# Optimization experiments

Hardware: AMD Instinct MI355X
Metric: run time of the kernel (lower is better)

## Reference

```python
import jax, jax.numpy as jnp
import numpy as np

D_MODEL = 16
NHEAD = 4
HEAD_DIM = D_MODEL // NHEAD
DFF = 64
NUM_LAYERS = 2
LN_EPS = 1e-5


def _layer_norm(x, w, b):
    mu = jnp.mean(x, axis=-1, keepdims=True)
    var = jnp.mean(jnp.square(x - mu), axis=-1, keepdims=True)
    return (x - mu) * jax.lax.rsqrt(var + LN_EPS) * w + b


def _encoder_layer(x, Wqkv, bqkv, Wo, bo, ln1w, ln1b, W1, b1, W2, b2, ln2w, ln2b):
    # x: [N, T, D]  (post-norm TransformerEncoderLayer, ReLU, no dropout)
    N, T, D = x.shape
    qkv = x @ Wqkv.T + bqkv                      # [N, T, 3D]
    q, k, v = jnp.split(qkv, 3, axis=-1)
    q = q.reshape(N, T, NHEAD, HEAD_DIM)
    k = k.reshape(N, T, NHEAD, HEAD_DIM)
    v = v.reshape(N, T, NHEAD, HEAD_DIM)
    scale = 1.0 / np.sqrt(HEAD_DIM)
    logits = jnp.einsum('nthd,nshd->nhts', q, k) * scale   # [N, H, T, T]
    attn = jax.nn.softmax(logits, axis=-1)
    ctx = jnp.einsum('nhts,nshd->nthd', attn, v).reshape(N, T, D)
    attn_out = ctx @ Wo.T + bo
    x = _layer_norm(x + attn_out, ln1w, ln1b)
    ff = jax.nn.relu(x @ W1.T + b1) @ W2.T + b2
    x = _layer_norm(x + ff, ln2w, ln2b)
    return x


def setup_inputs() -> dict:
    key = jax.random.key(0)
    ks = jax.random.split(key, 20)
    B, T, H, W = 1, 24, 256, 256
    L = NUM_LAYERS
    s = 0.05
    inp = {
        'x': jax.random.normal(ks[0], (B, T, H, W), dtype=jnp.float32),
        'Win': jax.random.normal(ks[1], (D_MODEL, 1), dtype=jnp.float32) * s,
        'bin': jnp.zeros((D_MODEL,), jnp.float32),
        'Wqkv': jax.random.normal(ks[2], (L, 3 * D_MODEL, D_MODEL), jnp.float32) * s,
        'bqkv': jnp.zeros((L, 3 * D_MODEL), jnp.float32),
        'Wo': jax.random.normal(ks[3], (L, D_MODEL, D_MODEL), jnp.float32) * s,
        'bo': jnp.zeros((L, D_MODEL), jnp.float32),
        'ln1w': jnp.ones((L, D_MODEL), jnp.float32),
        'ln1b': jnp.zeros((L, D_MODEL), jnp.float32),
        'W1': jax.random.normal(ks[4], (L, DFF, D_MODEL), jnp.float32) * s,
        'b1': jnp.zeros((L, DFF), jnp.float32),
        'W2': jax.random.normal(ks[5], (L, D_MODEL, DFF), jnp.float32) * s,
        'b2': jnp.zeros((L, D_MODEL), jnp.float32),
        'ln2w': jnp.ones((L, D_MODEL), jnp.float32),
        'ln2b': jnp.zeros((L, D_MODEL), jnp.float32),
        'Wout': jax.random.normal(ks[6], (1, D_MODEL), jnp.float32) * s,
        'bout': jnp.zeros((1,), jnp.float32),
    }
    return inp


def reference(x, Win, bin, Wqkv, bqkv, Wo, bo, ln1w, ln1b, W1, b1, W2, b2, ln2w, ln2b, Wout, bout):
    B, T, H, W = x.shape
    h = x.transpose(0, 2, 3, 1).reshape(B * H * W, T, 1)
    h = h @ Win.T + bin                              # [N, T, D]
    for l in range(NUM_LAYERS):
        h = _encoder_layer(h, Wqkv[l], bqkv[l], Wo[l], bo[l], ln1w[l], ln1b[l],
                           W1[l], b1[l], W2[l], b2[l], ln2w[l], ln2b[l])
    h = h @ Wout.T + bout                            # [N, T, 1]
    return h.reshape(B, H, W, T).transpose(0, 3, 1, 2)
```

## Files before the change

kernel.cpp:

```cpp
#include <hip/hip_runtime.h>
#include <hip/hip_bf16.h>


#define DM 16
#define NH 4
#define HD 4
#define TT 24
#define DFF 64
#define NSEQ 65536
#define SPB 8
#define BLK 192

typedef __fp16 h2_t  __attribute__((ext_vector_type(2)));
typedef __fp16 f16x4 __attribute__((ext_vector_type(4)));
typedef __fp16 f16x8 __attribute__((ext_vector_type(8)));
typedef float  f32x4 __attribute__((ext_vector_type(4)));

#define MFMA16(A,B,C) __builtin_amdgcn_mfma_f32_16x16x16f16(A,B,C,0,0,0)
#define LGKM0 asm volatile("s_waitcnt lgkmcnt(0)" ::: "memory")

#define OFF_WIN  0
#define OFF_BIN  16
#define OFF_WQKV 32
#define OFF_BQKV 1568
#define OFF_WO   1664
#define OFF_BO   2176
#define OFF_LN1W 2208
#define OFF_LN1B 2240
#define OFF_B1   2272
#define OFF_B2   2400
#define OFF_LN2W 2432
#define OFF_LN2B 2464
#define OFF_WOUT 2496
#define OFF_BOUT 2512
#define OFF_WQH  2516
#define OFF_WOH  3284
#define OFF_W1H  3540
#define OFF_W2H  4564
#define OFF_XBF  5588
#define OFF_DA   5592
#define OFF_WV   5608
#define OFF_W0   5672
#define NDW      5688

#define FOLD 0.7213475204444817f

#define KVS 97
#define TSTR 40

__device__ __forceinline__ float fdot2(h2_t a, h2_t b, float c) {
    return __builtin_amdgcn_fdot2(a, b, c, false);
}
__device__ __forceinline__ h2_t pkrn(float a, float b) {
    h2_t r; r[0] = (__fp16)a; r[1] = (__fp16)b; return r;
}

__device__ __forceinline__ int x_is_bf16(const unsigned* xw) {
    int ok = 1;
    #pragma unroll
    for (int i = 0; i < 32; ++i) {
        unsigned u = xw[i];
        unsigned e0 = (u >> 7)  & 0xFF;
        unsigned e1 = (u >> 23) & 0xFF;
        ok &= (e0 >= 64u) & (e0 <= 134u) & (e1 >= 64u) & (e1 <= 134u);
    }
    return ok;
}

__global__ __launch_bounds__(256) void cvt_params(
    const void* __restrict__ p0,  const void* __restrict__ p1,
    const void* __restrict__ p2,  const void* __restrict__ p3,
    const void* __restrict__ p4,  const void* __restrict__ p5,
    const void* __restrict__ p6,  const void* __restrict__ p7,
    const void* __restrict__ p8,  const void* __restrict__ p9,
    const void* __restrict__ p10, const void* __restrict__ p11,
    const void* __restrict__ p12, const void* __restrict__ p13,
    const void* __restrict__ p14, const void* __restrict__ p15,
    const void* __restrict__ px,
    float* __restrict__ ws)
{
    int i = blockIdx.x * 256 + threadIdx.x;
    if (i >= NDW) return;
    const int wbf = (((const unsigned*)p6)[0] == 0x3F803F80u);
    auto ld = [&](const void* p, int j) -> float {
        return wbf ? __bfloat162float(((const __hip_bfloat16*)p)[j])
                   : ((const float*)p)[j];
    };
    unsigned* wsu = (unsigned*)ws;
    auto st2 = [&](float a, float b) {
        union { h2_t h; unsigned u; } cv;
        cv.h = pkrn(a, b);
        wsu[i] = cv.u;
    };

    if      (i < OFF_BIN)  { ws[i] = ld(p0, i); }
    else if (i < OFF_WQKV) { ws[i] = ld(p1, i - OFF_BIN); }
    else if (i < OFF_BQKV) {
        int k = i - OFF_WQKV;
        int row = (k >> 4) % 48;
        float v = ld(p2, k);
        if (row < DM) v *= FOLD;
        ws[i] = v;
    }
    else if (i < OFF_WO) {
        int k = i - OFF_BQKV;
        float v = ld(p3, k);
        if (k % 48 < DM) v *= FOLD;
        ws[i] = v;
    }
    else if (i < OFF_BO)   { ws[i] = ld(p4,  i - OFF_WO);   }
    else if (i < OFF_LN1W) { ws[i] = ld(p5,  i - OFF_BO);   }
    else if (i < OFF_LN1B) { ws[i] = ld(p6,  i - OFF_LN1W); }
    else if (i < OFF_B1)   { ws[i] = ld(p7,  i - OFF_LN1B); }
    else if (i < OFF_B2)   { ws[i] = ld(p9,  i - OFF_B1);   }
    else if (i < OFF_LN2W) { ws[i] = ld(p11, i - OFF_B2);   }
    else if (i < OFF_LN2B) { ws[i] = ld(p12, i - OFF_LN2W); }
    else if (i < OFF_WOUT) { ws[i] = ld(p13, i - OFF_LN2B); }
    else if (i < OFF_BOUT) { ws[i] = ld(p14, i - OFF_WOUT); }
    else if (i < OFF_WQH)  { ws[i] = ld(p15, 0); }
    else if (i < OFF_WOH) {
        int k = i - OFF_WQH, l = k / 384, r = (k % 384) / 8, dp = k % 8;
        int j = l * 768 + r * 16 + 2 * dp;
        float s = (r < DM) ? FOLD : 1.f;
        st2(ld(p2, j) * s, ld(p2, j + 1) * s);
    }
    else if (i < OFF_W1H) {
        int k = i - OFF_WOH, l = k / 128, o = (k % 128) / 8, dp = k % 8;
        int j = l * 256 + o * 16 + 2 * dp;
        st2(ld(p4, j), ld(p4, j + 1));
    }
    else if (i < OFF_W2H) {
        int k = i - OFF_W1H, l = k / 512, f = (k % 512) / 8, dp = k % 8;
        int j = l * 1024 + f * 16 + 2 * dp;
        st2(ld(p8, j), ld(p8, j + 1));
    }
    else if (i < OFF_XBF) {
        int k = i - OFF_W2H, l = k / 512, r = k % 512, o = r / 32, fp = r % 32;
        int j = l * 1024 + o * 64 + 2 * fp;
        st2(ld(p10, j), ld(p10, j + 1));
    }
    else if (i < OFF_DA) {
        ws[i] = (i == OFF_XBF) ? (x_is_bf16((const unsigned*)px) ? 1.f : 0.f)
                               : 0.f;
    }
    else if (i < OFF_WV) {
        int k = i - OFF_DA, kind = k >> 2, hh = k & 3;
        float acc = 0.f;
        for (int j = hh * 4; j < hh * 4 + 4; ++j) {
            float qv;
            if (kind < 2) {
                qv = 0.f;
                for (int m = 0; m < 16; ++m) qv += ld(p2, j*16 + m) * ld(p0, m);
            } else {
                qv = ld(p3, j);
                for (int m = 0; m < 16; ++m) qv += ld(p2, j*16 + m) * ld(p1, m);
            }
            float kv;
            if ((kind & 1) == 0) {
                kv = 0.f;
                for (int m = 0; m < 16; ++m) kv += ld(p2, (16+j)*16 + m) * ld(p0, m);
            } else {
                kv = ld(p3, 16 + j);
                for (int m = 0; m < 16; ++m) kv += ld(p2, (16+j)*16 + m) * ld(p1, m);
            }
            acc += qv * kv;
        }
        ws[i] = acc * FOLD;
    }
    else if (i < OFF_W0) {
        int k = i - OFF_WV, o = k >> 2, hh = k & 3;
        float acc = 0.f;
        for (int j = hh * 4; j < hh * 4 + 4; ++j) {
            float vd = 0.f;
            for (int m = 0; m < 16; ++m) vd += ld(p2, (32+j)*16 + m) * ld(p0, m);
            acc += ld(p4, o*16 + j) * vd;
        }
        ws[i] = acc;
    }
    else {
        int o = i - OFF_W0;
        float acc = ld(p5, o);
        for (int j = 0; j < 16; ++j) {
            float vo = ld(p3, 32 + j);
            for (int m = 0; m < 16; ++m) vo += ld(p2, (32+j)*16 + m) * ld(p1, m);
            acc += ld(p4, o*16 + j) * vo;
        }
        ws[i] = acc;
    }
}


__device__ __forceinline__ void attn4(const float4* k4, const float4* v4,
                                      int base, const float* q, float* ctx) {
    #pragma unroll
    for (int hh = 0; hh < NH; ++hh) {
        const float qa = q[hh*4+0], qb = q[hh*4+1];
        const float qc = q[hh*4+2], qd = q[hh*4+3];
        float sum = 0.f, cx = 0.f, cy = 0.f, cz = 0.f, cw = 0.f;
        #pragma unroll
        for (int s = 0; s < TT; ++s) {
            float4 kk = k4[base + s * NH + hh];
            float e = __builtin_exp2f(qa*kk.x + qb*kk.y + qc*kk.z + qd*kk.w);
            float4 vv = v4[base + s * NH + hh];
            sum += e;
            cx += e*vv.x; cy += e*vv.y; cz += e*vv.z; cw += e*vv.w;
        }
        float inv = __builtin_amdgcn_rcpf(sum);
        ctx[hh*4+0] = cx*inv; ctx[hh*4+1] = cy*inv;
        ctx[hh*4+2] = cz*inv; ctx[hh*4+3] = cw*inv;
    }
}

__device__ __forceinline__ void ln16(const float* y, const float* w,
                                     const float* b, float* out) {
    float mu = 0.f;
    #pragma unroll
    for (int o = 0; o < DM; ++o) mu += y[o];
    mu *= (1.f / DM);
    float var = 0.f;
    #pragma unroll
    for (int o = 0; o < DM; ++o) { float z = y[o] - mu; var += z * z; }
    float r = rsqrtf(var * (1.f / DM) + 1e-5f);
    #pragma unroll
    for (int o = 0; o < DM; ++o) out[o] = (y[o] - mu) * r * w[o] + b[o];
}

__device__ __forceinline__ void stage_hi(const float* v, __fp16* slab, int lane) {
    #pragma unroll
    for (int m = 0; m < 4; ++m) {
        f16x4 p;
        #pragma unroll
        for (int j = 0; j < 4; ++j) p[j] = (__fp16)v[4*m+j];
        *(f16x4*)(slab + lane * TSTR + m * 8) = p;
    }
}

__device__ __forceinline__ void wo1(float* h, const float* ctx,
        const __fp16* Wh, const float* bo, const float* lw, const float* lb,
        __fp16* slab, int col, int grp, int lane)
{
    stage_hi(ctx, slab, lane);
    LGKM0;
    f16x4 B[4];
    #pragma unroll
    for (int m = 0; m < 4; ++m)
        B[m] = *(const f16x4*)(slab + (m*16 + col) * TSTR + grp * 8);
    LGKM0;
    f16x4 A = *(const f16x4*)(Wh + col * DM + grp * 4);
    f32x4 C = *(const f32x4*)(bo + grp * 4);
    #pragma unroll
    for (int m = 0; m < 4; ++m) {
        f32x4 d = MFMA16(A, B[m], C);
        f16x4 o4;
        #pragma unroll
        for (int j = 0; j < 4; ++j) o4[j] = (__fp16)d[j];
        *(f16x4*)(slab + (m*16 + col) * TSTR + grp * 8 + 4) = o4;
    }
    LGKM0;
    float y[DM];
    #pragma unroll
    for (int m = 0; m < 4; ++m) {
        f16x4 a = *(const f16x4*)(slab + lane * TSTR + m * 8 + 4);
        #pragma unroll
        for (int j = 0; j < 4; ++j) y[4*m+j] = h[4*m+j] + (float)a[j];
    }
    ln16(y, lw, lb, h);
}

__device__ __forceinline__ void ff_mfma(float* h, int col, int grp, int lane,
        const __fp16* W1h,
        const __fp16* W2h,
        const float* b1, const float* b2,
        const float* l2w, const float* l2b,
        __fp16* slab)
{
    stage_hi(h, slab, lane);
    LGKM0;
    f16x4 B1[4];
    #pragma unroll
    for (int m = 0; m < 4; ++m)
        B1[m] = *(const f16x4*)(slab + (m*16 + col) * TSTR + grp * 8);
    LGKM0;
    f16x4 A1[4], A2[4];
    f32x4 bb1[4];
    #pragma unroll
    for (int c = 0; c < 4; ++c) {
        A1[c]  = *(const f16x4*)(W1h + (c*16 + col)*16 + grp*4);
        A2[c]  = *(const f16x4*)(W2h + col*64 + c*16 + grp*4);
        bb1[c] = *(const f32x4*)(b1 + c*16 + grp*4);
    }
    const f32x4 b2f = *(const f32x4*)(b2 + grp*4);
    #pragma unroll
    for (int m = 0; m < 4; ++m) {
        f32x4 d1[4];
        #pragma unroll
        for (int c = 0; c < 4; ++c) d1[c] = MFMA16(A1[c], B1[m], bb1[c]);
        f16x4 u[4];
        #pragma unroll
        for (int c = 0; c < 4; ++c) {
            #pragma unroll
            for (int j = 0; j < 4; ++j)
                u[c][j] = (__fp16)fmaxf(d1[c][j], 0.f);
        }
        f32x4 d2 = b2f;
        #pragma unroll
        for (int c = 0; c < 4; ++c) d2 = MFMA16(A2[c], u[c], d2);
        f16x4 o4;
        #pragma unroll
        for (int j = 0; j < 4; ++j) o4[j] = (__fp16)d2[j];
        *(f16x4*)(slab + (m*16 + col) * TSTR + grp * 8 + 4) = o4;
    }
    LGKM0;
    float y[DM];
    #pragma unroll
    for (int m = 0; m < 4; ++m) {
        f16x4 a = *(const f16x4*)(slab + lane * TSTR + m * 8 + 4);
        #pragma unroll
        for (int j = 0; j < 4; ++j)
            y[4*m+j] = h[4*m+j] + (float)a[j];
    }
    ln16(y, l2w, l2b, h);
}

__global__ __launch_bounds__(BLK, 3) void tf_kernel(
    const void* __restrict__ xin,
    const float* __restrict__ P,
    void* __restrict__ outp)
{
    __shared__ float4 kvbuf[2 * SPB * KVS];
    __shared__ float  xs[SPB * 25];
    float4* k4 = kvbuf;
    float4* v4 = kvbuf + SPB * KVS;

    const __fp16* WqkvH = (const __fp16*)(P + OFF_WQH);
    const __fp16* WoHh  = (const __fp16*)(P + OFF_WOH);
    const __fp16* W1h   = (const __fp16*)(P + OFF_W1H);
    const __fp16* W2h   = (const __fp16*)(P + OFF_W2H);

    const int tid  = threadIdx.x;
    const int sl   = tid / TT;
    const int t    = tid % TT;
    const int n    = blockIdx.x * SPB + sl;
    const int idx  = t * NSEQ + n;
    const int base = sl * KVS;
    const int lane = tid & 63;
    const int wb   = tid & ~63;
    const int col  = lane & 15;
    const int grp  = lane >> 4;

    __fp16* slab = (__fp16*)kvbuf + (tid >> 6) * (64 * TSTR);

    const int xbf = (P[OFF_XBF] != 0.f);

    float xv;
    if (xbf) xv = __bfloat162float(((const __hip_bfloat16*)xin)[idx]);
    else     xv = ((const float*)xin)[idx];
    xs[sl * 25 + t] = xv;

    float h[DM];
    #pragma unroll
    for (int d = 0; d < DM; ++d)
        h[d] = xv * P[OFF_WIN + d] + P[OFF_BIN + d];
    __syncthreads();

    {
        float m1[NH];
        #pragma unroll
        for (int hh = 0; hh < NH; ++hh) {
            float f1 = P[OFF_DA + hh]     * xv + P[OFF_DA + 8  + hh];
            float f2 = P[OFF_DA + 4 + hh] * xv + P[OFF_DA + 12 + hh];
            float sum = 0.f, sxv = 0.f;
            #pragma unroll
            for (int s = 0; s < TT; ++s) {
                float xvs = xs[sl * 25 + s];
                float e = __builtin_exp2f(f1 * xvs + f2);
                sum += e;
                sxv += e * xvs;
            }
            m1[hh] = sxv * __builtin_amdgcn_rcpf(sum);
        }
        float y[DM];
        #pragma unroll
        for (int o = 0; o < DM; ++o) {
            f32x4 wv = *(const f32x4*)(P + OFF_WV + o * 4);
            y[o] = h[o] + P[OFF_W0 + o]
                 + m1[0]*wv[0] + m1[1]*wv[1] + m1[2]*wv[2] + m1[3]*wv[3];
        }
        ln16(y, P + OFF_LN1W, P + OFF_LN1B, h);

        ff_mfma(h, col, grp, lane, W1h, W2h,
                P + OFF_B1, P + OFF_B2, P + OFF_LN2W, P + OFF_LN2B, slab);
    }

    {
        const __fp16* WqH1 = WqkvH + 768;
        const float*  bq   = P + OFF_BQKV + 48;

        stage_hi(h, slab, lane);
        LGKM0;
        f16x4 B[4];
        #pragma unroll
        for (int m = 0; m < 4; ++m)
            B[m] = *(const f16x4*)(slab + (m*16 + col) * TSTR + grp * 8);
        f16x4 Ak = *(const f16x4*)(WqH1 + (16 + col) * DM + grp * 4);
        f16x4 Av = *(const f16x4*)(WqH1 + (32 + col) * DM + grp * 4);
        f32x4 Ck = *(const f32x4*)(bq + 16 + grp * 4);
        f32x4 Cv = *(const f32x4*)(bq + 32 + grp * 4);
        f32x4 dk[4], dv[4];
        #pragma unroll
        for (int m = 0; m < 4; ++m) {
            dk[m] = MFMA16(Ak, B[m], Ck);
            dv[m] = MFMA16(Av, B[m], Cv);
        }
        __syncthreads();
        #pragma unroll
        for (int m = 0; m < 4; ++m) {
            int bt = wb + m * 16 + col;
            int s2 = bt / TT, t2 = bt - s2 * TT;
            int ad = s2 * KVS + t2 * NH + grp;
            k4[ad] = make_float4(dk[m][0], dk[m][1], dk[m][2], dk[m][3]);
            v4[ad] = make_float4(dv[m][0], dv[m][1], dv[m][2], dv[m][3]);
        }

        h2_t h2[8];
        #pragma unroll
        for (int m = 0; m < 8; ++m) h2[m] = pkrn(h[2*m], h[2*m+1]);
        float q[DM];
        #pragma unroll
        for (int m = 0; m < 8; ++m) {
            float a0 = bq[2*m], a1 = bq[2*m+1];
            const h2_t* w0 = (const h2_t*)(WqH1 + (2*m) * DM);
            const h2_t* w1 = (const h2_t*)(WqH1 + (2*m+1) * DM);
            #pragma unroll
            for (int dp = 0; dp < 8; ++dp) {
                a0 = fdot2(h2[dp], w0[dp], a0);
                a1 = fdot2(h2[dp], w1[dp], a1);
            }
            q[2*m] = a0; q[2*m+1] = a1;
        }
        __syncthreads();

        float ctx[DM];
        attn4(k4, v4, base, q, ctx);
        __syncthreads();

        wo1(h, ctx, WoHh + 256, P + OFF_BO + 16,
            P + OFF_LN1W + 16, P + OFF_LN1B + 16, slab, col, grp, lane);

        ff_mfma(h, col, grp, lane, W1h + 1024, W2h + 1024,
                P + OFF_B1 + 64, P + OFF_B2 + 16,
                P + OFF_LN2W + 16, P + OFF_LN2B + 16, slab);
    }

    float a = P[OFF_BOUT];
    #pragma unroll
    for (int d = 0; d < DM; ++d)
        a += h[d] * P[OFF_WOUT + d];
    if (xbf) ((__hip_bfloat16*)outp)[idx] = __float2bfloat16(a);
    else     ((float*)outp)[idx] = a;
}

extern "C" void kernel_launch(void* const* d_in, const int* in_sizes, int n_in,
                              void* d_out, int out_size, void* d_ws, size_t ws_size,
                              hipStream_t stream) {
    float* P = (float*)d_ws;

    cvt_params<<<(NDW + 255) / 256, 256, 0, stream>>>(
        d_in[1],  d_in[2],  d_in[3],  d_in[4],
        d_in[5],  d_in[6],  d_in[7],  d_in[8],
        d_in[9],  d_in[10], d_in[11], d_in[12],
        d_in[13], d_in[14], d_in[15], d_in[16],
        d_in[0],
        P);

    tf_kernel<<<NSEQ / SPB, BLK, 0, stream>>>(d_in[0], P, d_out);
}
```

Baseline: 275.3 us.

## Store layer-2 K/V in fp16 and compute attention with packed fdot2

Layer-2 K and V are now kept in shared memory as fp16, transposed so each head's keys and values sit in contiguous vectors. Attention scores and the weighted sum over values are computed with packed fp16 dot products. This halves the shared-memory footprint and cuts ALU work, at the cost of fp16 rounding on the softmax weights and values. The final LayerNorm is also folded with the output projection into precomputed constants, conversions use the pkrtz instruction, and the layer-1 loop is reordered to interleave heads.

```diff
diff --git a/kernel.cpp b/kernel.cpp
--- a/kernel.cpp
+++ b/kernel.cpp
@@ -41,15 +41,26 @@
 #define OFF_DA   5592
 #define OFF_WV   5608
 #define OFF_W0   5672
-#define NDW      5688
+#define OFF_WP   5688
+#define OFF_C0   5704
+#define OFF_SWP  5705
+#define NDW      5706
 
 #define FOLD 0.7213475204444817f
 
-#define KVS 97
+#define KVH 196
 #define TSTR 40
 
 __device__ __forceinline__ float fdot2(h2_t a, h2_t b, float c) {
     return __builtin_amdgcn_fdot2(a, b, c, false);
+}
+__device__ __forceinline__ h2_t pkz(float a, float b) {
+    return __builtin_amdgcn_cvt_pkrtz(a, b);
+}
+__device__ __forceinline__ f16x4 pk4(float a, float b, float c, float d) {
+    union { h2_t h[2]; f16x4 v; } u;
+    u.h[0] = pkz(a, b); u.h[1] = pkz(c, d);
+    return u.v;
 }
 __device__ __forceinline__ h2_t pkrn(float a, float b) {
     h2_t r; r[0] = (__fp16)a; r[1] = (__fp16)b; return r;
@@ -177,7 +188,7 @@
         }
         ws[i] = acc;
     }
-    else {
+    else if (i < OFF_WP) {
         int o = i - OFF_W0;
         float acc = ld(p5, o);
         for (int j = 0; j < 16; ++j) {
@@ -187,29 +198,22 @@
         }
         ws[i] = acc;
     }
-}
-
-
-__device__ __forceinline__ void attn4(const float4* k4, const float4* v4,
-                                      int base, const float* q, float* ctx) {
-    #pragma unroll
-    for (int hh = 0; hh < NH; ++hh) {
-        const float qa = q[hh*4+0], qb = q[hh*4+1];
-        const float qc = q[hh*4+2], qd = q[hh*4+3];
-        float sum = 0.f, cx = 0.f, cy = 0.f, cz = 0.f, cw = 0.f;
-        #pragma unroll
-        for (int s = 0; s < TT; ++s) {
-            float4 kk = k4[base + s * NH + hh];
-            float e = __builtin_exp2f(qa*kk.x + qb*kk.y + qc*kk.z + qd*kk.w);
-            float4 vv = v4[base + s * NH + hh];
-            sum += e;
-            cx += e*vv.x; cy += e*vv.y; cz += e*vv.z; cw += e*vv.w;
-        }
-        float inv = __builtin_amdgcn_rcpf(sum);
-        ctx[hh*4+0] = cx*inv; ctx[hh*4+1] = cy*inv;
-        ctx[hh*4+2] = cz*inv; ctx[hh*4+3] = cw*inv;
-    }
-}
+    else if (i < OFF_C0) {
+        int o = i - OFF_WP;
+        ws[i] = ld(p14, o) * ld(p12, 16 + o);
+    }
+    else if (i == OFF_C0) {
+        float acc = ld(p15, 0);
+        for (int o = 0; o < 16; ++o) acc += ld(p14, o) * ld(p13, 16 + o);
+        ws[i] = acc;
+    }
+    else {
+        float acc = 0.f;
+        for (int o = 0; o < 16; ++o) acc += ld(p14, o) * ld(p12, 16 + o);
+        ws[i] = acc;
+    }
+}
+
 
 __device__ __forceinline__ void ln16(const float* y, const float* w,
                                      const float* b, float* out) {
@@ -225,56 +229,20 @@
     for (int o = 0; o < DM; ++o) out[o] = (y[o] - mu) * r * w[o] + b[o];
 }
 
-__device__ __forceinline__ void stage_hi(const float* v, __fp16* slab, int lane) {
-    #pragma unroll
-    for (int m = 0; m < 4; ++m) {
-        f16x4 p;
-        #pragma unroll
-        for (int j = 0; j < 4; ++j) p[j] = (__fp16)v[4*m+j];
-        *(f16x4*)(slab + lane * TSTR + m * 8) = p;
-    }
-}
-
-__device__ __forceinline__ void wo1(float* h, const float* ctx,
-        const __fp16* Wh, const float* bo, const float* lw, const float* lb,
-        __fp16* slab, int col, int grp, int lane)
-{
-    stage_hi(ctx, slab, lane);
-    LGKM0;
-    f16x4 B[4];
+__device__ __forceinline__ void stage_pk(const float* v, __fp16* slab, int lane) {
     #pragma unroll
     for (int m = 0; m < 4; ++m)
-        B[m] = *(const f16x4*)(slab + (m*16 + col) * TSTR + grp * 8);
-    LGKM0;
-    f16x4 A = *(const f16x4*)(Wh + col * DM + grp * 4);
-    f32x4 C = *(const f32x4*)(bo + grp * 4);
-    #pragma unroll
-    for (int m = 0; m < 4; ++m) {
-        f32x4 d = MFMA16(A, B[m], C);
-        f16x4 o4;
-        #pragma unroll
-        for (int j = 0; j < 4; ++j) o4[j] = (__fp16)d[j];
-        *(f16x4*)(slab + (m*16 + col) * TSTR + grp * 8 + 4) = o4;
-    }
-    LGKM0;
-    float y[DM];
-    #pragma unroll
-    for (int m = 0; m < 4; ++m) {
-        f16x4 a = *(const f16x4*)(slab + lane * TSTR + m * 8 + 4);
-        #pragma unroll
-        for (int j = 0; j < 4; ++j) y[4*m+j] = h[4*m+j] + (float)a[j];
-    }
-    ln16(y, lw, lb, h);
+        *(f16x4*)(slab + lane * TSTR + m * 8) =
+            pk4(v[4*m], v[4*m+1], v[4*m+2], v[4*m+3]);
 }
 
 __device__ __forceinline__ void ff_mfma(float* h, int col, int grp, int lane,
-        const __fp16* W1h,
-        const __fp16* W2h,
+        const __fp16* W1h, const __fp16* W2h,
         const float* b1, const float* b2,
         const float* l2w, const float* l2b,
         __fp16* slab)
 {
-    stage_hi(h, slab, lane);
+    stage_pk(h, slab, lane);
     LGKM0;
     f16x4 B1[4];
     #pragma unroll
@@ -295,20 +263,15 @@
         f32x4 d1[4];
         #pragma unroll
         for (int c = 0; c < 4; ++c) d1[c] = MFMA16(A1[c], B1[m], bb1[c]);
-        f16x4 u[4];
+        f32x4 d2 = b2f;
         #pragma unroll
         for (int c = 0; c < 4; ++c) {
-            #pragma unroll
-            for (int j = 0; j < 4; ++j)
-                u[c][j] = (__fp16)fmaxf(d1[c][j], 0.f);
-        }
-        f32x4 d2 = b2f;
-        #pragma unroll
-        for (int c = 0; c < 4; ++c) d2 = MFMA16(A2[c], u[c], d2);
-        f16x4 o4;
-        #pragma unroll
-        for (int j = 0; j < 4; ++j) o4[j] = (__fp16)d2[j];
-        *(f16x4*)(slab + (m*16 + col) * TSTR + grp * 8 + 4) = o4;
+            f16x4 u = pk4(fmaxf(d1[c][0], 0.f), fmaxf(d1[c][1], 0.f),
+                          fmaxf(d1[c][2], 0.f), fmaxf(d1[c][3], 0.f));
+            d2 = MFMA16(A2[c], u, d2);
+        }
+        *(f16x4*)(slab + (m*16 + col) * TSTR + grp * 8 + 4) =
+            pk4(d2[0], d2[1], d2[2], d2[3]);
     }
     LGKM0;
     float y[DM];
@@ -327,10 +290,11 @@
     const float* __restrict__ P,
     void* __restrict__ outp)
 {
-    __shared__ float4 kvbuf[2 * SPB * KVS];
-    __shared__ float  xs[SPB * 25];
-    float4* k4 = kvbuf;
-    float4* v4 = kvbuf + SPB * KVS;
+    __shared__ __align__(16) __fp16 shbuf[7680];
+    __shared__ float xs[SPB * 25];
+
+    h2_t* Kh = (h2_t*)shbuf;
+    h2_t* Vh = Kh + SPB * KVH;
 
     const __fp16* WqkvH = (const __fp16*)(P + OFF_WQH);
     const __fp16* WoHh  = (const __fp16*)(P + OFF_WOH);
@@ -342,13 +306,12 @@
     const int t    = tid % TT;
     const int n    = blockIdx.x * SPB + sl;
     const int idx  = t * NSEQ + n;
-    const int base = sl * KVS;
     const int lane = tid & 63;
     const int wb   = tid & ~63;
     const int col  = lane & 15;
     const int grp  = lane >> 4;
 
-    __fp16* slab = (__fp16*)kvbuf + (tid >> 6) * (64 * TSTR);
+    __fp16* slab = shbuf + (tid >> 6) * (64 * TSTR);
 
     const int xbf = (P[OFF_XBF] != 0.f);
 
@@ -364,21 +327,28 @@
     __syncthreads();
 
     {
+        float f1[NH], f2[NH], sum[NH], sxv[NH];
+        #pragma unroll
+        for (int hh = 0; hh < NH; ++hh) {
+            f1[hh] = P[OFF_DA + hh]     * xv + P[OFF_DA + 8  + hh];
+            f2[hh] = P[OFF_DA + 4 + hh] * xv + P[OFF_DA + 12 + hh];
+            sum[hh] = 0.f; sxv[hh] = 0.f;
+        }
+        #pragma unroll
+        for (int s = 0; s < TT; ++s) {
+            float xvs = xs[sl * 25 + s];
+            #pragma unroll
+            for (int hh = 0; hh < NH; ++hh) {
+                float e = __builtin_exp2f(f1[hh] * xvs + f2[hh]);
+                sum[hh] += e;
+                sxv[hh] += e * xvs;
+            }
+        }
         float m1[NH];
         #pragma unroll
-        for (int hh = 0; hh < NH; ++hh) {
-            float f1 = P[OFF_DA + hh]     * xv + P[OFF_DA + 8  + hh];
-            float f2 = P[OFF_DA + 4 + hh] * xv + P[OFF_DA + 12 + hh];
-            float sum = 0.f, sxv = 0.f;
-            #pragma unroll
-            for (int s = 0; s < TT; ++s) {
-                float xvs = xs[sl * 25 + s];
-                float e = __builtin_exp2f(f1 * xvs + f2);
-                sum += e;
-                sxv += e * xvs;
-            }
-            m1[hh] = sxv * __builtin_amdgcn_rcpf(sum);
-        }
+        for (int hh = 0; hh < NH; ++hh)
+            m1[hh] = sxv[hh] * __builtin_amdgcn_rcpf(sum[hh]);
+
         float y[DM];
         #pragma unroll
         for (int o = 0; o < DM; ++o) {
@@ -396,7 +366,7 @@
         const __fp16* WqH1 = WqkvH + 768;
         const float*  bq   = P + OFF_BQKV + 48;
 
-        stage_hi(h, slab, lane);
+        stage_pk(h, slab, lane);
         LGKM0;
         f16x4 B[4];
         #pragma unroll
@@ -417,15 +387,21 @@
         for (int m = 0; m < 4; ++m) {
             int bt = wb + m * 16 + col;
             int s2 = bt / TT, t2 = bt - s2 * TT;
-            int ad = s2 * KVS + t2 * NH + grp;
-            k4[ad] = make_float4(dk[m][0], dk[m][1], dk[m][2], dk[m][3]);
-            v4[ad] = make_float4(dv[m][0], dv[m][1], dv[m][2], dv[m][3]);
-        }
-
-        h2_t h2[8];
-        #pragma unroll
-        for (int m = 0; m < 8; ++m) h2[m] = pkrn(h[2*m], h[2*m+1]);
-        float q[DM];
+            union { h2_t h[2]; unsigned u[2]; } kk;
+            kk.h[0] = pkz(dk[m][0], dk[m][1]);
+            kk.h[1] = pkz(dk[m][2], dk[m][3]);
+            *(h2_t*)(Kh + s2 * KVH + grp * 48 + 2 * t2)     = kk.h[0];
+            *(h2_t*)(Kh + s2 * KVH + grp * 48 + 2 * t2 + 1) = kk.h[1];
+            __fp16* Vhh = (__fp16*)(Vh + s2 * KVH + grp * 48);
+            #pragma unroll
+            for (int j = 0; j < 4; ++j)
+                Vhh[j * 24 + t2] = (__fp16)dv[m][j];
+        }
+
+        h2_t h2v[8];
+        #pragma unroll
+        for (int m = 0; m < 8; ++m) h2v[m] = pkz(h[2*m], h[2*m+1]);
+        h2_t q2[8];
         #pragma unroll
         for (int m = 0; m < 8; ++m) {
             float a0 = bq[2*m], a1 = bq[2*m+1];
@@ -433,31 +409,141 @@
             const h2_t* w1 = (const h2_t*)(WqH1 + (2*m+1) * DM);
             #pragma unroll
             for (int dp = 0; dp < 8; ++dp) {
-                a0 = fdot2(h2[dp], w0[dp], a0);
-                a1 = fdot2(h2[dp], w1[dp], a1);
-            }
-            q[2*m] = a0; q[2*m+1] = a1;
+                a0 = fdot2(h2v[dp], w0[dp], a0);
+                a1 = fdot2(h2v[dp], w1[dp], a1);
+            }
+            q2[m] = pkz(a0, a1);
         }
         __syncthreads();
 
         float ctx[DM];
-        attn4(k4, v4, base, q, ctx);
+        h2_t one2; one2[0] = (__fp16)1.f; one2[1] = (__fp16)1.f;
+        #pragma unroll
+        for (int hh = 0; hh < NH; ++hh) {
+            const h2_t qa = q2[2*hh], qb = q2[2*hh+1];
+            const h2_t* Kp = Kh + sl * KVH + hh * 48;
+            h2_t e2[12];
+            float sum = 0.f;
+            #pragma unroll
+            for (int p = 0; p < 12; ++p) {
+                union { f16x8 v; h2_t h[4]; } kk;
+                kk.v = *(const f16x8*)(Kp + 4*p);
+                float d0 = fdot2(qb, kk.h[1], fdot2(qa, kk.h[0], 0.f));
+                float d1 = fdot2(qb, kk.h[3], fdot2(qa, kk.h[2], 0.f));
+                e2[p] = pkz(__builtin_exp2f(d0), __builtin_exp2f(d1));
+                sum = fdot2(e2[p], one2, sum);
+            }
+            float inv = __builtin_amdgcn_rcpf(sum);
+            const h2_t* Vp = Vh + sl * KVH + hh * 48;
+            #pragma unroll
+            for (int o = 0; o < 4; ++o) {
+                union { f16x8 v; h2_t h[4]; } v0, v1;
+                v0.v = *(const f16x8*)(Vp + o*12);
+                v1.v = *(const f16x8*)(Vp + o*12 + 4);
+                union { f16x4 v; h2_t h[2]; } v2;
+                v2.v = *(const f16x4*)(Vp + o*12 + 8);
+                float c = 0.f;
+                #pragma unroll
+                for (int p = 0; p < 4; ++p) c = fdot2(e2[p],     v0.h[p], c);
+                #pragma unroll
+                for (int p = 0; p < 4; ++p) c = fdot2(e2[4 + p], v1.h[p], c);
+                c = fdot2(e2[8], v2.h[0], c);
+                c = fdot2(e2[9], v2.h[1], c);
+                union { f16x4 v; h2_t h[2]; } v3;
+                v3.v = *(const f16x4*)(Vp + o*12 + 10);
+                c = fdot2(e2[10], v3.h[0], c);
+                c = fdot2(e2[11], v3.h[1], c);
+                ctx[hh*4 + o] = c * inv;
+            }
+        }
         __syncthreads();
 
-        wo1(h, ctx, WoHh + 256, P + OFF_BO + 16,
-            P + OFF_LN1W + 16, P + OFF_LN1B + 16, slab, col, grp, lane);
-
-        ff_mfma(h, col, grp, lane, W1h + 1024, W2h + 1024,
-                P + OFF_B1 + 64, P + OFF_B2 + 16,
-                P + OFF_LN2W + 16, P + OFF_LN2B + 16, slab);
-    }
-
-    float a = P[OFF_BOUT];
-    #pragma unroll
-    for (int d = 0; d < DM; ++d)
-        a += h[d] * P[OFF_WOUT + d];
-    if (xbf) ((__hip_bfloat16*)outp)[idx] = __float2bfloat16(a);
-    else     ((float*)outp)[idx] = a;
+        {
+            stage_pk(ctx, slab, lane);
+            LGKM0;
+            f16x4 Bc[4];
+            #pragma unroll
+            for (int m = 0; m < 4; ++m)
+                Bc[m] = *(const f16x4*)(slab + (m*16 + col) * TSTR + grp * 8);
+            LGKM0;
+            f16x4 A = *(const f16x4*)(WoHh + 256 + col * DM + grp * 4);
+            f32x4 C = *(const f32x4*)(P + OFF_BO + 16 + grp * 4);
+            #pragma unroll
+            for (int m = 0; m < 4; ++m) {
+                f32x4 d = MFMA16(A, Bc[m], C);
+                *(f16x4*)(slab + (m*16 + col) * TSTR + grp * 8 + 4) =
+                    pk4(d[0], d[1], d[2], d[3]);
+            }
+            LGKM0;
+            float y[DM];
+            #pragma unroll
+            for (int m = 0; m < 4; ++m) {
+                f16x4 a = *(const f16x4*)(slab + lane * TSTR + m * 8 + 4);
+                #pragma unroll
+                for (int j = 0; j < 4; ++j) y[4*m+j] = h[4*m+j] + (float)a[j];
+            }
+            ln16(y, P + OFF_LN1W + 16, P + OFF_LN1B + 16, h);
+        }
+
+        {
+            stage_pk(h, slab, lane);
+            LGKM0;
+            f16x4 B1[4];
+            #pragma unroll
+            for (int m = 0; m < 4; ++m)
+                B1[m] = *(const f16x4*)(slab + (m*16 + col) * TSTR + grp * 8);
+            LGKM0;
+            const __fp16* W1f = W1h + 1024;
+            const __fp16* W2f = W2h + 1024;
+            const float*  b1  = P + OFF_B1 + 64;
+            f16x4 A1[4], A2[4];
+            f32x4 bb1[4];
+            #pragma unroll
+            for (int c = 0; c < 4; ++c) {
+                A1[c]  = *(const f16x4*)(W1f + (c*16 + col)*16 + grp*4);
+                A2[c]  = *(const f16x4*)(W2f + col*64 + c*16 + grp*4);
+                bb1[c] = *(const f32x4*)(b1 + c*16 + grp*4);
+            }
+            const f32x4 b2f = *(const f32x4*)(P + OFF_B2 + 16 + grp*4);
+            #pragma unroll
+            for (int m = 0; m < 4; ++m) {
+                f32x4 d1[4];
+                #pragma unroll
+                for (int c = 0; c < 4; ++c) d1[c] = MFMA16(A1[c], B1[m], bb1[c]);
+                f32x4 d2 = b2f;
+                #pragma unroll
+                for (int c = 0; c < 4; ++c) {
+                    f16x4 u = pk4(fmaxf(d1[c][0], 0.f), fmaxf(d1[c][1], 0.f),
+                                  fmaxf(d1[c][2], 0.f), fmaxf(d1[c][3], 0.f));
+                    d2 = MFMA16(A2[c], u, d2);
+                }
+                *(f16x4*)(slab + (m*16 + col) * TSTR + grp * 8 + 4) =
+                    pk4(d2[0], d2[1], d2[2], d2[3]);
+            }
+            LGKM0;
+            float y[DM];
+            #pragma unroll
+            for (int m = 0; m < 4; ++m) {
+                f16x4 a = *(const f16x4*)(slab + lane * TSTR + m * 8 + 4);
+                #pragma unroll
+                for (int j = 0; j < 4; ++j) y[4*m+j] = h[4*m+j] + (float)a[j];
+            }
+            float mu = 0.f;
+            #pragma unroll
+            for (int o = 0; o < DM; ++o) mu += y[o];
+            mu *= (1.f / DM);
+            float var = 0.f;
+            #pragma unroll
+            for (int o = 0; o < DM; ++o) { float z = y[o] - mu; var += z * z; }
+            float r = rsqrtf(var * (1.f / DM) + 1e-5f);
+            float dotv = 0.f;
+            #pragma unroll
+            for (int o = 0; o < DM; ++o) dotv += P[OFF_WP + o] * y[o];
+            float outv = P[OFF_C0] + r * (dotv - mu * P[OFF_SWP]);
+            if (xbf) ((__hip_bfloat16*)outp)[idx] = __float2bfloat16(outv);
+            else     ((float*)outp)[idx] = outv;
+        }
+    }
 }
 
 extern "C" void kernel_launch(void* const* d_in, const int* in_sizes, int n_in,
```

Result: faster. 261.9 us (-4.9%).
